# Kernel tuning notes

Measured on AMD Instinct MI355X. Metric: run time of the kernel, lower is better.

## Reference

```python
import jax, jax.numpy as jnp
import numpy as np

DIM = 1024
HID = 2 * DIM
NUM_EXPERTS = 8
TOP_K = 2
BATCH, SEQ = 2, 2048


def setup_inputs() -> dict:
    key = jax.random.key(0)
    ks = jax.random.split(key, 8)
    s = 0.02
    return {
        "x": jax.random.normal(ks[0], (BATCH, SEQ, DIM), jnp.float32),
        "router_w": jax.random.normal(ks[1], (DIM, NUM_EXPERTS), jnp.float32) * s,
        "router_b": jnp.zeros((NUM_EXPERTS,), jnp.float32),
        "sw1": jax.random.normal(ks[2], (DIM, HID), jnp.float32) * s,
        "sb1": jnp.zeros((HID,), jnp.float32),
        "sw2": jax.random.normal(ks[3], (HID, DIM), jnp.float32) * s,
        "sb2": jnp.zeros((DIM,), jnp.float32),
        "ew1": jax.random.normal(ks[4], (NUM_EXPERTS, DIM, HID), jnp.float32) * s,
        "eb1": jnp.zeros((NUM_EXPERTS, HID), jnp.float32),
        "ew2": jax.random.normal(ks[5], (NUM_EXPERTS, HID, DIM), jnp.float32) * s,
        "eb2": jnp.zeros((NUM_EXPERTS, DIM), jnp.float32),
    }


def _gelu(x):
    # torch nn.GELU default is the exact (erf) form
    return jax.nn.gelu(x, approximate=False)


def reference(x, router_w, router_b, sw1, sb1, sw2, sb2, ew1, eb1, ew2, eb2):
    B, S, D = x.shape
    flat = x.reshape(-1, D)                      # [T, D]
    T = flat.shape[0]

    # Router: softmax -> top-k -> renormalize
    probs = jax.nn.softmax(flat @ router_w + router_b, axis=-1)  # [T, E]
    top_w, top_i = jax.lax.top_k(probs, TOP_K)                   # [T, K]
    top_w = top_w / jnp.sum(top_w, axis=-1, keepdims=True)
    # Dense per-token combine weights [T, E] (zero for unrouted experts)
    comb = jnp.zeros_like(probs).at[jnp.arange(T)[:, None], top_i].set(top_w)

    # Shared expert (always on)
    shared = _gelu(flat @ sw1 + sb1) @ sw2 + sb2                 # [T, D]

    # All experts as one batched GEMM pair; zero weights kill unrouted tokens.
    h = _gelu(jnp.einsum('td,edh->eth', flat, ew1) + eb1[:, None, :])  # [E, T, H]
    eo = jnp.einsum('eth,ehd->etd', h, ew2) + eb2[:, None, :]          # [E, T, D]
    moe = jnp.einsum('te,etd->td', comb, eo)                           # [T, D]

    return (shared + moe).reshape(B, S, D)
```

## Files before the change

kernel.cpp:

```cpp
#include <hip/hip_runtime.h>

#define DIM   1024
#define HID   2048
#define NE    8
#define T_TOK 4096

typedef __attribute__((ext_vector_type(8))) short short8;
typedef __attribute__((ext_vector_type(4))) float f32x4;

__device__ __forceinline__ ushort f2bf(float f) {
    union { float f; unsigned u; } v; v.f = f;
    unsigned r = v.u + 0x7FFFu + ((v.u >> 16) & 1u);
    return (ushort)(r >> 16);
}

__device__ __forceinline__ float gelu_fast(float x) {
    float t = x * x;
    float u = x * (1.0f + 0.044715f * t);
    float e = exp2f(2.3020585f * u);
    return x - x / (e + 1.0f);
}

__global__ void transpose_conv9(const float* __restrict__ ew, const float* __restrict__ sw,
                                ushort* __restrict__ ewT, ushort* __restrict__ swT,
                                int R, int C) {
    __shared__ float tile[32][65];
    int z = blockIdx.z;
    const float* in = (z < NE) ? ew + (size_t)z * R * C : sw;
    ushort* out     = (z < NE) ? ewT + (size_t)z * R * C : swT;
    int c0 = blockIdx.x * 32, r0 = blockIdx.y * 64;
    int tx = threadIdx.x & 31, ty = threadIdx.x >> 5;
#pragma unroll
    for (int rr = 0; rr < 64; rr += 8)
        tile[tx][rr + ty] = in[(size_t)(r0 + rr + ty) * C + (c0 + tx)];
    __syncthreads();
    int lane = threadIdx.x & 63, q = threadIdx.x >> 6;
#pragma unroll
    for (int j = 0; j < 8; ++j) {
        int cc = q * 8 + j;
        out[(size_t)(c0 + cc) * R + (r0 + lane)] = f2bf(tile[cc][lane]);
    }
}

__global__ void router_kernel(const float* __restrict__ x, const float* __restrict__ rw,
                              const float* __restrict__ rb, int* __restrict__ cnt,
                              int* __restrict__ ids, float* __restrict__ wts,
                              int* __restrict__ te, int* __restrict__ tp,
                              ushort* __restrict__ xb) {
    int wave = threadIdx.x >> 6;
    int lane = threadIdx.x & 63;
    int t = blockIdx.x * 4 + wave;
    const float* xr = x + (size_t)t * DIM;
    ushort* xo = xb + (size_t)t * DIM;
    float acc[NE];
#pragma unroll
    for (int e = 0; e < NE; ++e) acc[e] = 0.f;
    {
        int d0 = lane * 16;
        float v[16];
#pragma unroll
        for (int j = 0; j < 16; j += 4) {
            float4 f = *(const float4*)(xr + d0 + j);
            v[j] = f.x; v[j+1] = f.y; v[j+2] = f.z; v[j+3] = f.w;
        }
        short8 o0, o1;
#pragma unroll
        for (int j = 0; j < 8; ++j) { o0[j] = (short)f2bf(v[j]); o1[j] = (short)f2bf(v[8+j]); }
        *(short8*)(xo + d0)     = o0;
        *(short8*)(xo + d0 + 8) = o1;
#pragma unroll
        for (int j = 0; j < 16; ++j) {
#pragma unroll
            for (int e = 0; e < NE; ++e) acc[e] += v[j] * rw[(d0 + j) * NE + e];
        }
    }
#pragma unroll
    for (int e = 0; e < NE; ++e) {
#pragma unroll
        for (int off = 32; off; off >>= 1) acc[e] += __shfl_xor(acc[e], off);
    }
    if (lane == 0) {
        float l[NE];
#pragma unroll
        for (int e = 0; e < NE; ++e) l[e] = acc[e] + rb[e];
        int i1 = 0;
#pragma unroll
        for (int e = 1; e < NE; ++e) if (l[e] > l[i1]) i1 = e;
        int i2 = (i1 == 0) ? 1 : 0;
#pragma unroll
        for (int e = 0; e < NE; ++e) if (e != i1 && l[e] > l[i2]) i2 = e;
        float p2 = __expf(l[i2] - l[i1]);
        float w1 = 1.0f / (1.0f + p2);
        float w2 = p2 / (1.0f + p2);
        int pos1 = atomicAdd(&cnt[i1], 1);
        ids[i1 * T_TOK + pos1] = t; wts[i1 * T_TOK + pos1] = w1;
        te[2 * t] = i1; tp[2 * t] = pos1;
        int pos2 = atomicAdd(&cnt[i2], 1);
        ids[i2 * T_TOK + pos2] = t; wts[i2 * T_TOK + pos2] = w2;
        te[2 * t + 1] = i2; tp[2 * t + 1] = pos2;
    }
}

__global__ void build_queue(const int* __restrict__ cnt, int* __restrict__ offs,
                            int* __restrict__ q1, int* __restrict__ q2,
                            int* __restrict__ nq) {
    if (threadIdx.x != 0) return;
    int s = 0;
    for (int e = 0; e < NE; ++e) { offs[e] = s; s += cnt[e]; }
    int k1 = 0, k2 = 0;
    for (int z = 0; z <= NE; ++z) {
        int c = (z < NE) ? cnt[z] : T_TOK;
        int mts = (c + 127) >> 7;
        for (int mt = 0; mt < mts; ++mt) {
            for (int nt = 0; nt < HID / 128; ++nt)
                q1[k1++] = (z << 16) | (mt << 8) | nt;
            for (int nt = 0; nt < DIM / 128; ++nt)
                q2[k2++] = (z << 16) | (mt << 8) | nt;
        }
    }
    nq[0] = k1; nq[1] = k2;
    nq[2] = 0;  nq[3] = 0;
}

__device__ __forceinline__ void mma_tile(
    const ushort* __restrict__ A, const int* __restrict__ gather, int count,
    const ushort* __restrict__ BT, int K, int tileM, int tileN,
    ushort* lds, f32x4 acc[4][4])
{
    const int tid  = threadIdx.x;
    const int lane = tid & 63, wave = tid >> 6;
    const int g = lane >> 4, fr = lane & 15;
    const int swl = (fr & 7) << 3;
    const int sub = lane >> 3;
    const int kcs = ((lane & 7) ^ sub) << 3;
    const int wr = wave >> 1, wc = wave & 1;

    const ushort* asrc[4];
    const ushort* bsrc[4];
#pragma unroll
    for (int i = 0; i < 4; ++i) {
        int row = (wave * 4 + i) * 8 + sub;
        int ar = tileM + row; if (ar > count - 1) ar = count - 1;
        int grow = gather ? gather[ar] : ar;
        asrc[i] = A  + (size_t)grow * K + kcs;
        bsrc[i] = BT + (size_t)(tileN + row) * K + kcs;
    }

    const int NT = K >> 6;
    for (int t = 0; t < NT; ++t) {
#pragma unroll
        for (int i = 0; i < 4; ++i) {
            int chunk = wave * 4 + i;
            __builtin_amdgcn_global_load_lds(
                (const __attribute__((address_space(1))) void*)(asrc[i] + t * 64),
                (__attribute__((address_space(3))) void*)(lds + chunk * 512),
                16, 0, 0);
            __builtin_amdgcn_global_load_lds(
                (const __attribute__((address_space(1))) void*)(bsrc[i] + t * 64),
                (__attribute__((address_space(3))) void*)(lds + 8192 + chunk * 512),
                16, 0, 0);
        }
        __syncthreads();
#pragma unroll
        for (int kk = 0; kk < 2; ++kk) {
            int koff = (kk * 32 + g * 8) ^ swl;
            short8 a[4], b[4];
#pragma unroll
            for (int m = 0; m < 4; ++m) {
                int row = wr * 64 + m * 16 + fr;
                a[m] = *(const short8*)&lds[row * 64 + koff];
            }
#pragma unroll
            for (int n = 0; n < 4; ++n) {
                int col = wc * 64 + n * 16 + fr;
                b[n] = *(const short8*)&lds[8192 + col * 64 + koff];
            }
#pragma unroll
            for (int m = 0; m < 4; ++m)
#pragma unroll
                for (int n = 0; n < 4; ++n)
                    acc[m][n] = __builtin_amdgcn_mfma_f32_16x16x32_bf16(
                        a[m], b[n], acc[m][n], 0, 0, 0);
        }
        __syncthreads();
    }
}

__global__ __launch_bounds__(256, 4)
void gemm1_kernel(const ushort* __restrict__ xb,
                  const ushort* __restrict__ ew1T, const ushort* __restrict__ sw1T,
                  const float* __restrict__ eb1, const float* __restrict__ sb1,
                  const int* __restrict__ ids, const int* __restrict__ cnt,
                  const int* __restrict__ offs,
                  const int* __restrict__ q1, const int* __restrict__ nq,
                  int* __restrict__ qc, ushort* __restrict__ h)
{
    __shared__ ushort lds[16384];
    __shared__ int s_it;
    const int nit = nq[0];
    const int lane = threadIdx.x & 63, wave = threadIdx.x >> 6;
    const int wr = wave >> 1, wc = wave & 1, g = lane >> 4, fr = lane & 15;

    for (;;) {
        if (threadIdx.x == 0) s_it = atomicAdd(qc, 1);
        __syncthreads();
        int it = s_it;
        if (it >= nit) break;
        int item = q1[it];
        int z = item >> 16, mt = (item >> 8) & 255, nt = item & 255;
        int count, hbase;
        const ushort* BT; const float* bias; const int* gather;
        if (z < NE) {
            count  = cnt[z];
            BT     = ew1T + (size_t)z * HID * DIM;
            bias   = eb1 + z * HID;
            gather = ids + z * T_TOK;
            hbase  = T_TOK + offs[z];
        } else {
            count = T_TOK; BT = sw1T; bias = sb1; gather = nullptr; hbase = 0;
        }
        int tileM = mt * 128, tileN = nt * 128;

        f32x4 acc[4][4];
#pragma unroll
        for (int m = 0; m < 4; ++m)
#pragma unroll
            for (int n = 0; n < 4; ++n) acc[m][n] = (f32x4){0.f, 0.f, 0.f, 0.f};

        mma_tile(xb, gather, count, BT, DIM, tileM, tileN, lds, acc);

#pragma unroll
        for (int n = 0; n < 4; ++n) {
            int col = tileN + wc * 64 + n * 16 + fr;
            float bc = bias[col];
#pragma unroll
            for (int m = 0; m < 4; ++m) {
#pragma unroll
                for (int i = 0; i < 4; ++i) {
                    int row = tileM + wr * 64 + m * 16 + g * 4 + i;
                    if (row < count)
                        h[(size_t)(hbase + row) * HID + col] =
                            f2bf(gelu_fast(acc[m][n][i] + bc));
                }
            }
        }
    }
}

__global__ __launch_bounds__(256, 4)
void gemm2_kernel(const ushort* __restrict__ h,
                  const ushort* __restrict__ ew2T, const ushort* __restrict__ sw2T,
                  const float* __restrict__ eb2, const float* __restrict__ sb2,
                  const float* __restrict__ wts,
                  const int* __restrict__ cnt, const int* __restrict__ offs,
                  const int* __restrict__ q2, const int* __restrict__ nq,
                  int* __restrict__ qc, float* __restrict__ eo, float* __restrict__ out)
{
    __shared__ ushort lds[16384];
    __shared__ int s_it;
    const int nit = nq[1];
    const int lane = threadIdx.x & 63, wave = threadIdx.x >> 6;
    const int wr = wave >> 1, wc = wave & 1, g = lane >> 4, fr = lane & 15;

    for (;;) {
        if (threadIdx.x == 0) s_it = atomicAdd(qc, 1);
        __syncthreads();
        int it = s_it;
        if (it >= nit) break;
        int item = q2[it];
        int z = item >> 16, mt = (item >> 8) & 255, nt = item & 255;
        int count;
        const ushort* BT; const float* bias; const float* tw; float* dst;
        const ushort* Arows;
        if (z < NE) {
            count = cnt[z];
            BT    = ew2T + (size_t)z * DIM * HID;
            bias  = eb2 + z * DIM;
            tw    = wts + z * T_TOK;
            Arows = h + (size_t)(T_TOK + offs[z]) * HID;
            dst   = eo + (size_t)offs[z] * DIM;
        } else {
            count = T_TOK; BT = sw2T; bias = sb2; tw = nullptr;
            Arows = h;
            dst   = out;
        }
        int tileM = mt * 128, tileN = nt * 128;

        f32x4 acc[4][4];
#pragma unroll
        for (int m = 0; m < 4; ++m)
#pragma unroll
            for (int n = 0; n < 4; ++n) acc[m][n] = (f32x4){0.f, 0.f, 0.f, 0.f};

        mma_tile(Arows, nullptr, count, BT, HID, tileM, tileN, lds, acc);

#pragma unroll
        for (int m = 0; m < 4; ++m) {
#pragma unroll
            for (int i = 0; i < 4; ++i) {
                int row = tileM + wr * 64 + m * 16 + g * 4 + i;
                if (row < count) {
                    float w = tw ? tw[row] : 1.0f;
#pragma unroll
                    for (int n = 0; n < 4; ++n) {
                        int col = tileN + wc * 64 + n * 16 + fr;
                        dst[(size_t)row * DIM + col] = w * (acc[m][n][i] + bias[col]);
                    }
                }
            }
        }
    }
}

__global__ void combine_kernel(const float* __restrict__ eo, const int* __restrict__ te,
                               const int* __restrict__ tp, const int* __restrict__ offs,
                               float* __restrict__ out)
{
    int t = blockIdx.x;
    int s1 = offs[te[2 * t]]     + tp[2 * t];
    int s2 = offs[te[2 * t + 1]] + tp[2 * t + 1];
    int d = threadIdx.x * 4;
    float4 a = *(const float4*)(out + (size_t)t * DIM + d);
    float4 b = *(const float4*)(eo + (size_t)s1 * DIM + d);
    float4 c = *(const float4*)(eo + (size_t)s2 * DIM + d);
    a.x += b.x + c.x; a.y += b.y + c.y; a.z += b.z + c.z; a.w += b.w + c.w;
    *(float4*)(out + (size_t)t * DIM + d) = a;
}

extern "C" void kernel_launch(void* const* d_in, const int* in_sizes, int n_in,
                              void* d_out, int out_size, void* d_ws, size_t ws_size,
                              hipStream_t stream)
{
    const float* x   = (const float*)d_in[0];
    const float* rw  = (const float*)d_in[1];
    const float* rb  = (const float*)d_in[2];
    const float* sw1 = (const float*)d_in[3];
    const float* sb1 = (const float*)d_in[4];
    const float* sw2 = (const float*)d_in[5];
    const float* sb2 = (const float*)d_in[6];
    const float* ew1 = (const float*)d_in[7];
    const float* eb1 = (const float*)d_in[8];
    const float* ew2 = (const float*)d_in[9];
    const float* eb2 = (const float*)d_in[10];
    float* out = (float*)d_out;

    char* p = (char*)d_ws;
    ushort* xb   = (ushort*)p;  p += (size_t)T_TOK * DIM * 2;
    ushort* sw1T = (ushort*)p;  p += (size_t)HID * DIM * 2;
    ushort* sw2T = (ushort*)p;  p += (size_t)DIM * HID * 2;
    ushort* ew1T = (ushort*)p;  p += (size_t)NE * HID * DIM * 2;
    ushort* ew2T = (ushort*)p;  p += (size_t)NE * DIM * HID * 2;
    ushort* hbuf = (ushort*)p;  p += (size_t)(3 * T_TOK) * HID * 2;
    float*  eo   = (float*)p;   p += (size_t)(2 * T_TOK) * DIM * 4;
    int*    ids  = (int*)p;     p += (size_t)NE * T_TOK * 4;
    float*  wts  = (float*)p;   p += (size_t)NE * T_TOK * 4;
    int*    te   = (int*)p;     p += (size_t)2 * T_TOK * 4;
    int*    tp   = (int*)p;     p += (size_t)2 * T_TOK * 4;
    int*    cnt  = (int*)p;     p += 256;
    int*    offs = (int*)p;     p += 256;
    int*    q1   = (int*)p;     p += 16384;
    int*    q2   = (int*)p;     p += 8192;
    int*    nq   = (int*)p;     p += 256;

    hipMemsetAsync(cnt, 0, 256, stream);

    router_kernel<<<dim3(T_TOK / 4), 256, 0, stream>>>(x, rw, rb, cnt, ids, wts, te, tp, xb);
    transpose_conv9<<<dim3(HID / 32, DIM / 64, NE + 1), 256, 0, stream>>>(
        ew1, sw1, ew1T, sw1T, DIM, HID);
    transpose_conv9<<<dim3(DIM / 32, HID / 64, NE + 1), 256, 0, stream>>>(
        ew2, sw2, ew2T, sw2T, HID, DIM);
    build_queue<<<dim3(1), 64, 0, stream>>>(cnt, offs, q1, q2, nq);
    gemm1_kernel<<<dim3(1024), 256, 0, stream>>>(
        xb, ew1T, sw1T, eb1, sb1, ids, cnt, offs, q1, nq, nq + 2, hbuf);
    gemm2_kernel<<<dim3(1024), 256, 0, stream>>>(
        hbuf, ew2T, sw2T, eb2, sb2, wts, cnt, offs, q2, nq, nq + 3, eo, out);
    combine_kernel<<<dim3(T_TOK), 256, 0, stream>>>(eo, te, tp, offs, out);
}
```

Baseline: 368.1 us.

## Use 256x256 double-buffered GEMM2 tiles, fuse weight transposes, store expert outputs in bf16

GEMM2 moves to 512-thread blocks computing 256x256 tiles. Each tile is staged into 128KB of dynamic LDS with double-buffered global_load_lds, so loads overlap the MFMA work. The two weight transpose/convert launches are merged into one vectorized kernel with 64x64 tiles. Expert outputs are written as bf16 instead of fp32, which halves eo traffic in GEMM2 and the combine step. The work queue order is also changed to N-major, which should improve weight reuse in cache. The trade-offs are fewer resident blocks per CU, a larger register footprint, and added rounding error in the expert contributions.

```diff
diff --git a/kernel.cpp b/kernel.cpp
--- a/kernel.cpp
+++ b/kernel.cpp
@@ -12,6 +12,9 @@
     union { float f; unsigned u; } v; v.f = f;
     unsigned r = v.u + 0x7FFFu + ((v.u >> 16) & 1u);
     return (ushort)(r >> 16);
+}
+__device__ __forceinline__ float bf2f(ushort u) {
+    union { unsigned u; float f; } v; v.u = (unsigned)u << 16; return v.f;
 }
 
 __device__ __forceinline__ float gelu_fast(float x) {
@@ -21,24 +24,45 @@
     return x - x / (e + 1.0f);
 }
 
-__global__ void transpose_conv9(const float* __restrict__ ew, const float* __restrict__ sw,
-                                ushort* __restrict__ ewT, ushort* __restrict__ swT,
-                                int R, int C) {
-    __shared__ float tile[32][65];
+__global__ __launch_bounds__(256)
+void transpose_conv18(const float* __restrict__ ew1, const float* __restrict__ sw1,
+                      const float* __restrict__ ew2, const float* __restrict__ sw2,
+                      ushort* __restrict__ ew1T, ushort* __restrict__ sw1T,
+                      ushort* __restrict__ ew2T, ushort* __restrict__ sw2T) {
+    __shared__ float tile[64][65];
     int z = blockIdx.z;
-    const float* in = (z < NE) ? ew + (size_t)z * R * C : sw;
-    ushort* out     = (z < NE) ? ewT + (size_t)z * R * C : swT;
-    int c0 = blockIdx.x * 32, r0 = blockIdx.y * 64;
-    int tx = threadIdx.x & 31, ty = threadIdx.x >> 5;
-#pragma unroll
-    for (int rr = 0; rr < 64; rr += 8)
-        tile[tx][rr + ty] = in[(size_t)(r0 + rr + ty) * C + (c0 + tx)];
+    const float* in; ushort* out; int R, C, bx, by;
+    if (z < 9) {
+        R = DIM; C = HID; bx = blockIdx.x; by = blockIdx.y;
+        in  = (z < 8) ? ew1  + (size_t)z * R * C : sw1;
+        out = (z < 8) ? ew1T + (size_t)z * R * C : sw1T;
+    } else {
+        int zz = z - 9;
+        R = HID; C = DIM;
+        bx = blockIdx.x & 15; by = blockIdx.y * 2 + (blockIdx.x >> 4);
+        in  = (zz < 8) ? ew2  + (size_t)zz * R * C : sw2;
+        out = (zz < 8) ? ew2T + (size_t)zz * R * C : sw2T;
+    }
+    int c0 = bx * 64, r0 = by * 64;
+    int t = threadIdx.x;
+    int lr = t >> 4, lc4 = (t & 15) * 4;
+#pragma unroll
+    for (int p = 0; p < 4; ++p) {
+        float4 f = *(const float4*)(in + (size_t)(r0 + p * 16 + lr) * C + c0 + lc4);
+        tile[p * 16 + lr][lc4]     = f.x;
+        tile[p * 16 + lr][lc4 + 1] = f.y;
+        tile[p * 16 + lr][lc4 + 2] = f.z;
+        tile[p * 16 + lr][lc4 + 3] = f.w;
+    }
     __syncthreads();
-    int lane = threadIdx.x & 63, q = threadIdx.x >> 6;
-#pragma unroll
-    for (int j = 0; j < 8; ++j) {
-        int cc = q * 8 + j;
-        out[(size_t)(c0 + cc) * R + (r0 + lane)] = f2bf(tile[cc][lane]);
+    int oc = t >> 3, rg = (t & 7) * 8;
+#pragma unroll
+    for (int p = 0; p < 2; ++p) {
+        int c = p * 32 + oc;
+        short8 o;
+#pragma unroll
+        for (int j = 0; j < 8; ++j) o[j] = (short)f2bf(tile[rg + j][c]);
+        *(short8*)(out + (size_t)(c0 + c) * R + r0 + rg) = o;
     }
 }
 
@@ -110,13 +134,14 @@
     int k1 = 0, k2 = 0;
     for (int z = 0; z <= NE; ++z) {
         int c = (z < NE) ? cnt[z] : T_TOK;
-        int mts = (c + 127) >> 7;
-        for (int mt = 0; mt < mts; ++mt) {
-            for (int nt = 0; nt < HID / 128; ++nt)
+        int mts1 = (c + 127) >> 7;
+        for (int nt = 0; nt < HID / 128; ++nt)
+            for (int mt = 0; mt < mts1; ++mt)
                 q1[k1++] = (z << 16) | (mt << 8) | nt;
-            for (int nt = 0; nt < DIM / 128; ++nt)
+        int mts2 = (c + 255) >> 8;
+        for (int nt = 0; nt < DIM / 256; ++nt)
+            for (int mt = 0; mt < mts2; ++mt)
                 q2[k2++] = (z << 16) | (mt << 8) | nt;
-        }
     }
     nq[0] = k1; nq[1] = k2;
     nq[2] = 0;  nq[3] = 0;
@@ -183,6 +208,89 @@
                         a[m], b[n], acc[m][n], 0, 0, 0);
         }
         __syncthreads();
+    }
+}
+
+__device__ __forceinline__ void mma256(
+    const ushort* __restrict__ A, int count,
+    const ushort* __restrict__ BT, int K, int tileM, int tileN,
+    ushort* lds, f32x4 acc[8][4])
+{
+    const int tid  = threadIdx.x;
+    const int lane = tid & 63, wave = tid >> 6;
+    const int wr = wave >> 2, wc = wave & 3;
+    const int g = lane >> 4, fr = lane & 15;
+    const int swl = (fr & 7) << 3;
+    const int sub = lane >> 3;
+    const int kcs = ((lane & 7) ^ sub) << 3;
+
+    const ushort* asrc[4];
+    const ushort* bsrc[4];
+#pragma unroll
+    for (int i = 0; i < 4; ++i) {
+        int row = (wave * 4 + i) * 8 + sub;
+        int ar = tileM + row; if (ar > count - 1) ar = count - 1;
+        asrc[i] = A  + (size_t)ar * K + kcs;
+        bsrc[i] = BT + (size_t)(tileN + row) * K + kcs;
+    }
+
+    auto STAGE = [&](int buf, int t) {
+        ushort* base = lds + buf * 32768;
+#pragma unroll
+        for (int i = 0; i < 4; ++i) {
+            int chunk = wave * 4 + i;
+            __builtin_amdgcn_global_load_lds(
+                (const __attribute__((address_space(1))) void*)(asrc[i] + t * 64),
+                (__attribute__((address_space(3))) void*)(base + chunk * 512),
+                16, 0, 0);
+            __builtin_amdgcn_global_load_lds(
+                (const __attribute__((address_space(1))) void*)(bsrc[i] + t * 64),
+                (__attribute__((address_space(3))) void*)(base + 16384 + chunk * 512),
+                16, 0, 0);
+        }
+    };
+
+    auto COMPUTE = [&](int buf) {
+        const ushort* A_s = lds + buf * 32768;
+        const ushort* B_s = A_s + 16384;
+#pragma unroll
+        for (int kk = 0; kk < 2; ++kk) {
+            int koff = (kk * 32 + g * 8) ^ swl;
+            short8 a[8], b[4];
+#pragma unroll
+            for (int m = 0; m < 8; ++m) {
+                int row = wr * 128 + m * 16 + fr;
+                a[m] = *(const short8*)&A_s[row * 64 + koff];
+            }
+#pragma unroll
+            for (int n = 0; n < 4; ++n) {
+                int col = wc * 64 + n * 16 + fr;
+                b[n] = *(const short8*)&B_s[col * 64 + koff];
+            }
+#pragma unroll
+            for (int m = 0; m < 8; ++m)
+#pragma unroll
+                for (int n = 0; n < 4; ++n)
+                    acc[m][n] = __builtin_amdgcn_mfma_f32_16x16x32_bf16(
+                        a[m], b[n], acc[m][n], 0, 0, 0);
+        }
+    };
+
+    const int NT = K >> 6;
+    STAGE(0, 0);
+    for (int t = 0; t < NT; ++t) {
+        int cur = t & 1;
+        if (t + 1 < NT) {
+            STAGE(cur ^ 1, t + 1);
+            asm volatile("s_waitcnt vmcnt(8)" ::: "memory");
+        } else {
+            asm volatile("s_waitcnt vmcnt(0)" ::: "memory");
+        }
+        __builtin_amdgcn_s_barrier();
+        asm volatile("" ::: "memory");
+        COMPUTE(cur);
+        asm volatile("" ::: "memory");
+        __builtin_amdgcn_s_barrier();
     }
 }
 
@@ -247,20 +355,20 @@
     }
 }
 
-__global__ __launch_bounds__(256, 4)
+__global__ __launch_bounds__(512, 2)
 void gemm2_kernel(const ushort* __restrict__ h,
                   const ushort* __restrict__ ew2T, const ushort* __restrict__ sw2T,
                   const float* __restrict__ eb2, const float* __restrict__ sb2,
                   const float* __restrict__ wts,
                   const int* __restrict__ cnt, const int* __restrict__ offs,
                   const int* __restrict__ q2, const int* __restrict__ nq,
-                  int* __restrict__ qc, float* __restrict__ eo, float* __restrict__ out)
+                  int* __restrict__ qc, ushort* __restrict__ eo, float* __restrict__ out)
 {
-    __shared__ ushort lds[16384];
+    extern __shared__ ushort lds[];
     __shared__ int s_it;
     const int nit = nq[1];
     const int lane = threadIdx.x & 63, wave = threadIdx.x >> 6;
-    const int wr = wave >> 1, wc = wave & 1, g = lane >> 4, fr = lane & 15;
+    const int wr = wave >> 2, wc = wave & 3, g = lane >> 4, fr = lane & 15;
 
     for (;;) {
         if (threadIdx.x == 0) s_it = atomicAdd(qc, 1);
@@ -270,7 +378,7 @@
         int item = q2[it];
         int z = item >> 16, mt = (item >> 8) & 255, nt = item & 255;
         int count;
-        const ushort* BT; const float* bias; const float* tw; float* dst;
+        const ushort* BT; const float* bias; const float* tw;
         const ushort* Arows;
         if (z < NE) {
             count = cnt[z];
@@ -278,41 +386,59 @@
             bias  = eb2 + z * DIM;
             tw    = wts + z * T_TOK;
             Arows = h + (size_t)(T_TOK + offs[z]) * HID;
-            dst   = eo + (size_t)offs[z] * DIM;
         } else {
             count = T_TOK; BT = sw2T; bias = sb2; tw = nullptr;
             Arows = h;
-            dst   = out;
-        }
-        int tileM = mt * 128, tileN = nt * 128;
-
-        f32x4 acc[4][4];
-#pragma unroll
-        for (int m = 0; m < 4; ++m)
+        }
+        int tileM = mt * 256, tileN = nt * 256;
+
+        f32x4 acc[8][4];
+#pragma unroll
+        for (int m = 0; m < 8; ++m)
 #pragma unroll
             for (int n = 0; n < 4; ++n) acc[m][n] = (f32x4){0.f, 0.f, 0.f, 0.f};
 
-        mma_tile(Arows, nullptr, count, BT, HID, tileM, tileN, lds, acc);
-
-#pragma unroll
-        for (int m = 0; m < 4; ++m) {
-#pragma unroll
-            for (int i = 0; i < 4; ++i) {
-                int row = tileM + wr * 64 + m * 16 + g * 4 + i;
-                if (row < count) {
-                    float w = tw ? tw[row] : 1.0f;
-#pragma unroll
-                    for (int n = 0; n < 4; ++n) {
-                        int col = tileN + wc * 64 + n * 16 + fr;
-                        dst[(size_t)row * DIM + col] = w * (acc[m][n][i] + bias[col]);
+        mma256(Arows, count, BT, HID, tileM, tileN, lds, acc);
+
+        if (z < NE) {
+            ushort* dst = eo + (size_t)offs[z] * DIM;
+#pragma unroll
+            for (int m = 0; m < 8; ++m) {
+#pragma unroll
+                for (int i = 0; i < 4; ++i) {
+                    int row = tileM + wr * 128 + m * 16 + g * 4 + i;
+                    if (row < count) {
+                        float w = tw[row];
+#pragma unroll
+                        for (int n = 0; n < 4; ++n) {
+                            int col = tileN + wc * 64 + n * 16 + fr;
+                            dst[(size_t)row * DIM + col] =
+                                f2bf(w * (acc[m][n][i] + bias[col]));
+                        }
                     }
                 }
             }
-        }
-    }
-}
-
-__global__ void combine_kernel(const float* __restrict__ eo, const int* __restrict__ te,
+        } else {
+#pragma unroll
+            for (int m = 0; m < 8; ++m) {
+#pragma unroll
+                for (int i = 0; i < 4; ++i) {
+                    int row = tileM + wr * 128 + m * 16 + g * 4 + i;
+                    if (row < count) {
+#pragma unroll
+                        for (int n = 0; n < 4; ++n) {
+                            int col = tileN + wc * 64 + n * 16 + fr;
+                            out[(size_t)row * DIM + col] = acc[m][n][i] + bias[col];
+                        }
+                    }
+                }
+            }
+        }
+        __syncthreads();
+    }
+}
+
+__global__ void combine_kernel(const ushort* __restrict__ eo, const int* __restrict__ te,
                                const int* __restrict__ tp, const int* __restrict__ offs,
                                float* __restrict__ out)
 {
@@ -321,9 +447,12 @@
     int s2 = offs[te[2 * t + 1]] + tp[2 * t + 1];
     int d = threadIdx.x * 4;
     float4 a = *(const float4*)(out + (size_t)t * DIM + d);
-    float4 b = *(const float4*)(eo + (size_t)s1 * DIM + d);
-    float4 c = *(const float4*)(eo + (size_t)s2 * DIM + d);
-    a.x += b.x + c.x; a.y += b.y + c.y; a.z += b.z + c.z; a.w += b.w + c.w;
+    ushort4 b = *(const ushort4*)(eo + (size_t)s1 * DIM + d);
+    ushort4 c = *(const ushort4*)(eo + (size_t)s2 * DIM + d);
+    a.x += bf2f(b.x) + bf2f(c.x);
+    a.y += bf2f(b.y) + bf2f(c.y);
+    a.z += bf2f(b.z) + bf2f(c.z);
+    a.w += bf2f(b.w) + bf2f(c.w);
     *(float4*)(out + (size_t)t * DIM + d) = a;
 }
 
@@ -351,7 +480,7 @@
     ushort* ew1T = (ushort*)p;  p += (size_t)NE * HID * DIM * 2;
     ushort* ew2T = (ushort*)p;  p += (size_t)NE * DIM * HID * 2;
     ushort* hbuf = (ushort*)p;  p += (size_t)(3 * T_TOK) * HID * 2;
-    float*  eo   = (float*)p;   p += (size_t)(2 * T_TOK) * DIM * 4;
+    ushort* eo   = (ushort*)p;  p += (size_t)(2 * T_TOK) * DIM * 2;
     int*    ids  = (int*)p;     p += (size_t)NE * T_TOK * 4;
     float*  wts  = (float*)p;   p += (size_t)NE * T_TOK * 4;
     int*    te   = (int*)p;     p += (size_t)2 * T_TOK * 4;
@@ -362,17 +491,18 @@
     int*    q2   = (int*)p;     p += 8192;
     int*    nq   = (int*)p;     p += 256;
 
+    hipFuncSetAttribute((const void*)gemm2_kernel,
+                        hipFuncAttributeMaxDynamicSharedMemorySize, 131072);
+
     hipMemsetAsync(cnt, 0, 256, stream);
 
     router_kernel<<<dim3(T_TOK / 4), 256, 0, stream>>>(x, rw, rb, cnt, ids, wts, te, tp, xb);
-    transpose_conv9<<<dim3(HID / 32, DIM / 64, NE + 1), 256, 0, stream>>>(
-        ew1, sw1, ew1T, sw1T, DIM, HID);
-    transpose_conv9<<<dim3(DIM / 32, HID / 64, NE + 1), 256, 0, stream>>>(
-        ew2, sw2, ew2T, sw2T, HID, DIM);
+    transpose_conv18<<<dim3(32, 16, 18), 256, 0, stream>>>(
+        ew1, sw1, ew2, sw2, ew1T, sw1T, ew2T, sw2T);
     build_queue<<<dim3(1), 64, 0, stream>>>(cnt, offs, q1, q2, nq);
     gemm1_kernel<<<dim3(1024), 256, 0, stream>>>(
         xb, ew1T, sw1T, eb1, sb1, ids, cnt, offs, q1, nq, nq + 2, hbuf);
-    gemm2_kernel<<<dim3(1024), 256, 0, stream>>>(
+    gemm2_kernel<<<dim3(256), 512, 131072, stream>>>(
         hbuf, ew2T, sw2T, eb2, sb2, wts, cnt, offs, q2, nq, nq + 3, eo, out);
     combine_kernel<<<dim3(T_TOK), 256, 0, stream>>>(eo, te, tp, offs, out);
 }
```

After: 502.1 us. +36.4%, slower.
